# Kernel tuning notes

Hardware: AMD Instinct MI355X
Metric: run time of the kernel (lower is better)

## Reference

```python
import jax, jax.numpy as jnp
import numpy as np

K_H, K_W = 3, 3
STRIDE, PAD = 1, 1
GN_GROUPS = 32
EPS = 1e-5


def setup_inputs() -> dict:
    key = jax.random.key(0)
    k1, k2, k3 = jax.random.split(key, 3)
    B, C, H, W = 4, 256, 64, 64
    Cout = 256
    x = jax.random.normal(k1, (B, C, H, W), jnp.float32)
    offset = jax.random.normal(k2, (B, 2 * K_H * K_W, H, W), jnp.float32)
    weight = jax.random.normal(k3, (Cout, C, K_H, K_W), jnp.float32) * 0.02
    gamma = jnp.ones((Cout,), jnp.float32)
    beta = jnp.zeros((Cout,), jnp.float32)
    return {"x": x, "offset": offset, "weight": weight, "gamma": gamma, "beta": beta}


def _deform_conv(x, offset, weight):
    B, C, H, W = x.shape
    Cout = weight.shape[0]
    K = K_H * K_W
    Ho = (H + 2 * PAD - K_H) // STRIDE + 1
    Wo = (W + 2 * PAD - K_W) // STRIDE + 1
    ky, kx = jnp.meshgrid(jnp.arange(K_H), jnp.arange(K_W), indexing='ij')
    ky = ky.reshape(K).astype(x.dtype)
    kx = kx.reshape(K).astype(x.dtype)
    # base sampling positions per kernel tap
    py_base = (jnp.arange(Ho) * STRIDE - PAD).astype(x.dtype)[None, :] + ky[:, None]  # [K,Ho]
    px_base = (jnp.arange(Wo) * STRIDE - PAD).astype(x.dtype)[None, :] + kx[:, None]  # [K,Wo]
    off = offset.reshape(B, K, 2, Ho, Wo)  # mmcv layout: (dy, dx) pairs per tap
    py = py_base[None, :, :, None] + off[:, :, 0]  # [B,K,Ho,Wo]
    px = px_base[None, :, None, :] + off[:, :, 1]  # [B,K,Ho,Wo]
    y0 = jnp.floor(py)
    x0 = jnp.floor(px)
    ly = py - y0
    lx = px - x0
    xf = x.reshape(B, C, H * W)

    def gather(yi, xi):
        valid = (yi >= 0) & (yi <= H - 1) & (xi >= 0) & (xi <= W - 1)
        yc = jnp.clip(yi, 0, H - 1).astype(jnp.int32)
        xc = jnp.clip(xi, 0, W - 1).astype(jnp.int32)
        idx = yc * W + xc  # [B,K,Ho,Wo]
        vals = jax.vmap(lambda xb, ib: xb[:, ib])(xf, idx)  # [B,C,K,Ho,Wo]
        return vals * valid[:, None].astype(x.dtype)

    g00 = gather(y0, x0)
    g01 = gather(y0, x0 + 1)
    g10 = gather(y0 + 1, x0)
    g11 = gather(y0 + 1, x0 + 1)
    wy = ly[:, None]  # [B,1,K,Ho,Wo]
    wx = lx[:, None]
    val = ((1 - wy) * (1 - wx) * g00 + (1 - wy) * wx * g01
           + wy * (1 - wx) * g10 + wy * wx * g11)  # [B,C,K,Ho,Wo]
    return jnp.einsum('bckhw,ock->bohw', val, weight.reshape(Cout, C, K))


def reference(x, offset, weight, gamma, beta):
    y = _deform_conv(x, offset, weight)  # [B,Cout,Ho,Wo]
    B, C, H, W = y.shape
    yg = y.reshape(B, GN_GROUPS, C // GN_GROUPS, H, W)
    mean = jnp.mean(yg, axis=(2, 3, 4), keepdims=True)
    var = jnp.var(yg, axis=(2, 3, 4), keepdims=True)
    yn = ((yg - mean) * jax.lax.rsqrt(var + EPS)).reshape(B, C, H, W)
    out = yn * gamma[None, :, None, None] + beta[None, :, None, None]
    return jax.nn.relu(out)
```

## Files before the change

### kernel.cpp

```cpp
#include <hip/hip_runtime.h>

typedef unsigned short ushort_t;
typedef __bf16 bf16x8 __attribute__((ext_vector_type(8)));
typedef float f32x4 __attribute__((ext_vector_type(4)));
typedef void __attribute__((address_space(1))) gvoid_t;
typedef void __attribute__((address_space(3))) lvoid_t;

__device__ __forceinline__ float bflo(unsigned u) { return __builtin_bit_cast(float, u << 16); }
__device__ __forceinline__ float bfhi(unsigned u) { return __builtin_bit_cast(float, u & 0xffff0000u); }
__device__ __forceinline__ unsigned f2bf_bits(float f) {
  unsigned u = __builtin_bit_cast(unsigned, f);
  return (u + 0x7fffu + ((u >> 16) & 1u)) >> 16;
}
__device__ __forceinline__ ushort_t f2bf(float f) { return (ushort_t)f2bf_bits(f); }

#define VMWAIT(N) asm volatile("s_waitcnt vmcnt(" #N ")" ::: "memory")
#define LGKM0 asm volatile("s_waitcnt lgkmcnt(0)" ::: "memory")

__global__ __launch_bounds__(256) void k_prep_w(const float* __restrict__ w,
                                                ushort_t* __restrict__ wb) {
  const int idx = blockIdx.x * 256 + threadIdx.x;
  const float* src = w + (size_t)idx * 9;
  #pragma unroll
  for (int k = 0; k < 9; ++k)
    wb[(k << 16) + idx] = f2bf(src[k]);
}

__global__ __launch_bounds__(256) void k_prep_x(const float* __restrict__ x,
                                                ushort_t* __restrict__ xt) {
  __shared__ ushort_t tile[64][68];
  const int bid = blockIdx.x;
  const int b = bid >> 8;
  const int ct = (bid >> 6) & 3;
  const int pt = bid & 63;
  const int t = threadIdx.x;
  const float* xb = x + ((size_t)(b * 256 + ct * 64)) * 4096 + pt * 64;
  #pragma unroll
  for (int i = 0; i < 16; ++i) {
    const int idx = t + 256 * i;
    const int c_l = idx >> 6, p_l = idx & 63;
    tile[c_l][p_l] = f2bf(xb[(size_t)c_l * 4096 + p_l]);
  }
  __syncthreads();
  ushort_t* xo = xt + ((size_t)(b * 4096 + pt * 64)) * 256 + ct * 64;
  #pragma unroll
  for (int i = 0; i < 16; ++i) {
    const int idx = t + 256 * i;
    const int p_l = idx >> 6, c_l = idx & 63;
    xo[(size_t)p_l * 256 + c_l] = tile[c_l][p_l];
  }
}

struct SMeta {
  float w00, w01, w10, w11;
  int i00, i01, i10, i11;
};
__device__ __forceinline__ SMeta meta_for(int h, int gw, int k, float oy, float ox) {
  SMeta m;
  const float py = (float)(h - 1 + k / 3) + oy;
  const float px = (float)(gw - 1 + k % 3) + ox;
  const float fy = floorf(py), fx = floorf(px);
  const float ly = py - fy, lx = px - fx;
  const int iy0 = (int)fy, ix0 = (int)fx;
  const float vy0 = (iy0 >= 0 && iy0 < 64) ? 1.f : 0.f;
  const float vy1 = (iy0 >= -1 && iy0 < 63) ? 1.f : 0.f;
  const float vx0 = (ix0 >= 0 && ix0 < 64) ? 1.f : 0.f;
  const float vx1 = (ix0 >= -1 && ix0 < 63) ? 1.f : 0.f;
  m.w00 = (1.f - ly) * (1.f - lx) * vy0 * vx0;
  m.w01 = (1.f - ly) * lx * vy0 * vx1;
  m.w10 = ly * (1.f - lx) * vy1 * vx0;
  m.w11 = ly * lx * vy1 * vx1;
  const int cy0 = min(max(iy0, 0), 63), cy1 = min(max(iy0 + 1, 0), 63);
  const int cx0 = min(max(ix0, 0), 63), cx1 = min(max(ix0 + 1, 0), 63);
  m.i00 = (cy0 * 64 + cx0) * 256;
  m.i01 = (cy0 * 64 + cx1) * 256;
  m.i10 = (cy1 * 64 + cx0) * 256;
  m.i11 = (cy1 * 64 + cx1) * 256;
  return m;
}

__device__ __forceinline__ unsigned lerp_pack(unsigned a, unsigned b, unsigned c, unsigned d,
                                              float w00, float w01, float w10, float w11) {
  float lo = w00 * bflo(a) + w01 * bflo(b) + w10 * bflo(c) + w11 * bflo(d);
  float hi = w00 * bfhi(a) + w01 * bfhi(b) + w10 * bfhi(c) + w11 * bfhi(d);
  return f2bf_bits(lo) | (f2bf_bits(hi) << 16);
}

__global__ __launch_bounds__(512) void k_gemm(const float* __restrict__ off,
                                              const ushort_t* __restrict__ xt,
                                              const ushort_t* __restrict__ wb,
                                              float* __restrict__ y,
                                              float* __restrict__ stats) {
  __shared__ __attribute__((aligned(16))) ushort_t Abuf[2][64 * 64];
  __shared__ __attribute__((aligned(16))) ushort_t Bbuf[3][256 * 64];

  const int bid = blockIdx.x;
  const int lb = ((bid & 7) << 5) | (bid >> 3);
  const int b = lb >> 6;
  const int h = lb & 63;
  const int t = threadIdx.x;
  const int wave = t >> 6;
  const int lane = t & 63;
  const int wq = lane >> 4;
  const int wr = lane & 15;
  const int wm = wave >> 2;
  const int wn = wave & 3;

  const int s_w = t >> 3;
  const int c8 = t & 7;

  const f32x4 zero = {0.f, 0.f, 0.f, 0.f};
  f32x4 acc[2][4];
  #pragma unroll
  for (int i = 0; i < 2; ++i)
    #pragma unroll
    for (int j = 0; j < 4; ++j) acc[i][j] = zero;

  const ushort_t* xtb = xt + (size_t)b * 4096 * 256;

  float oy[9], ox[9];
  {
    const float* offb = off + (size_t)b * 18 * 4096 + h * 64 + s_w;
    #pragma unroll
    for (int k = 0; k < 9; ++k) {
      oy[k] = offb[(2 * k) * 4096];
      ox[k] = offb[(2 * k + 1) * 4096];
    }
  }

#define GATHER_ISSUE(TAP, C0)                             \
  {                                                       \
    m = meta_for(h, s_w, (TAP), oy[(TAP)], ox[(TAP)]);    \
    const int cc = (C0) + c8 * 8;                         \
    q00 = *(const uint4*)(xtb + m.i00 + cc);              \
    q01 = *(const uint4*)(xtb + m.i01 + cc);              \
    q10 = *(const uint4*)(xtb + m.i10 + cc);              \
    q11 = *(const uint4*)(xtb + m.i11 + cc);              \
  }

#define B_ISSUE(TAP, C0, BUF)                                                                \
  {                                                                                          \
    _Pragma("unroll") for (int i_ = 0; i_ < 4; ++i_) {                                       \
      const int idx_ = i_ * 512 + t;                                                         \
      const int row_ = idx_ >> 3, slot_ = idx_ & 7;                                          \
      const ushort_t* g_ = wb + ((TAP) << 16) + row_ * 256 + (C0) + ((slot_ ^ (row_ & 7)) << 3); \
      __builtin_amdgcn_global_load_lds((gvoid_t*)g_,                                         \
                                       (lvoid_t*)((char*)&Bbuf[(BUF)][0] + idx_ * 16), 16,   \
                                       0, 0);                                                \
    }                                                                                        \
  }

#define A_WRITE(BUF)                                                         \
  {                                                                          \
    uint4 r;                                                                 \
    r.x = lerp_pack(q00.x, q01.x, q10.x, q11.x, m.w00, m.w01, m.w10, m.w11); \
    r.y = lerp_pack(q00.y, q01.y, q10.y, q11.y, m.w00, m.w01, m.w10, m.w11); \
    r.z = lerp_pack(q00.z, q01.z, q10.z, q11.z, m.w00, m.w01, m.w10, m.w11); \
    r.w = lerp_pack(q00.w, q01.w, q10.w, q11.w, m.w00, m.w01, m.w10, m.w11); \
    *(uint4*)&Abuf[(BUF)][s_w * 64 + ((c8 ^ (s_w & 7)) << 3)] = r;           \
  }

  {
    uint4 q00, q01, q10, q11;
    SMeta m;
    GATHER_ISSUE(0, 0);
    B_ISSUE(0, 0, 0);
    B_ISSUE(0, 64, 1);
    VMWAIT(8);
    A_WRITE(0);
    LGKM0;
    __builtin_amdgcn_s_barrier();
  }

  #pragma unroll
  for (int n = 0; n < 36; ++n) {
    const int curB = n % 3;
    const int curA = n & 1;
    uint4 q00, q01, q10, q11;
    SMeta m;
    if (n < 35) {
      GATHER_ISSUE((n + 1) >> 2, ((n + 1) & 3) << 6);
    }
    if (n < 34) {
      B_ISSUE((n + 2) >> 2, ((n + 2) & 3) << 6, (n + 2) % 3);
    }
    VMWAIT(12);
    #pragma unroll
    for (int ks = 0; ks < 2; ++ks) {
      bf16x8 af[2], bfr[4];
      #pragma unroll
      for (int tm = 0; tm < 2; ++tm) {
        const int row = wm * 32 + tm * 16 + wr;
        const int slot = (ks * 4 + wq) ^ (row & 7);
        af[tm] = *(const bf16x8*)&Abuf[curA][row * 64 + slot * 8];
      }
      #pragma unroll
      for (int tn = 0; tn < 4; ++tn) {
        const int row = wn * 64 + tn * 16 + wr;
        const int slot = (ks * 4 + wq) ^ (row & 7);
        bfr[tn] = *(const bf16x8*)&Bbuf[curB][row * 64 + slot * 8];
      }
      #pragma unroll
      for (int tm = 0; tm < 2; ++tm)
        #pragma unroll
        for (int tn = 0; tn < 4; ++tn)
          acc[tm][tn] =
              __builtin_amdgcn_mfma_f32_16x16x32_bf16(af[tm], bfr[tn], acc[tm][tn], 0, 0, 0);
    }
    if (n < 35) {
      if (n == 34) {
        VMWAIT(0);
      } else {
        VMWAIT(4);
      }
      A_WRITE((n + 1) & 1);
      LGKM0;
      __builtin_amdgcn_s_barrier();
    }
  }
#undef GATHER_ISSUE
#undef B_ISSUE
#undef A_WRITE

  float* yb = y + ((size_t)(b * 4096 + h * 64)) * 256;
  #pragma unroll
  for (int tm = 0; tm < 2; ++tm) {
    #pragma unroll
    for (int tn = 0; tn < 4; ++tn) {
      const int o = wn * 64 + tn * 16 + wr;
      #pragma unroll
      for (int r2 = 0; r2 < 4; ++r2) {
        const int ww = wm * 32 + tm * 16 + wq * 4 + r2;
        yb[ww * 256 + o] = acc[tm][tn][r2];
      }
    }
  }
  #pragma unroll
  for (int tn = 0; tn < 4; ++tn) {
    float sum = 0.f, ss = 0.f;
    #pragma unroll
    for (int tm = 0; tm < 2; ++tm)
      #pragma unroll
      for (int r2 = 0; r2 < 4; ++r2) {
        const float v = acc[tm][tn][r2];
        sum += v;
        ss += v * v;
      }
    sum += __shfl_xor(sum, 16, 64);
    ss += __shfl_xor(ss, 16, 64);
    sum += __shfl_xor(sum, 32, 64);
    ss += __shfl_xor(ss, 32, 64);
    #pragma unroll
    for (int d = 1; d < 8; d <<= 1) {
      sum += __shfl_xor(sum, d, 64);
      ss += __shfl_xor(ss, d, 64);
    }
    if (wq == 0 && (wr & 7) == 0) {
      const int gi = wn * 8 + tn * 2 + (wr >> 3);
      atomicAdd(&stats[(b * 32 + gi) * 2], sum);
      atomicAdd(&stats[(b * 32 + gi) * 2 + 1], ss);
    }
  }
}

__global__ __launch_bounds__(256) void k_apply(const float* __restrict__ y,
                                               const float* __restrict__ stats,
                                               const float* __restrict__ gamma,
                                               const float* __restrict__ beta,
                                               float* __restrict__ out) {
  __shared__ float tile[64][65];
  __shared__ float sm[8], sr[8], sg[64], sb[64];
  const int bid = blockIdx.x;
  const int lb = ((bid & 7) << 7) | (bid >> 3);
  const int b = lb >> 8;
  const int st = (lb >> 2) & 63;
  const int ot = lb & 3;
  const int t = threadIdx.x;
  if (t < 8) {
    const int g = ot * 8 + t;
    const float s1 = stats[(b * 32 + g) * 2];
    const float s2 = stats[(b * 32 + g) * 2 + 1];
    const float mean = s1 * (1.f / 32768.f);
    const float var = s2 * (1.f / 32768.f) - mean * mean;
    sm[t] = mean;
    sr[t] = rsqrtf(var + 1e-5f);
  }
  if (t < 64) {
    sg[t] = gamma[ot * 64 + t];
    sb[t] = beta[ot * 64 + t];
  }
  const float* yb = y + ((size_t)(b * 4096 + st * 64)) * 256 + ot * 64;
  #pragma unroll
  for (int i = 0; i < 16; ++i) {
    const int idx = t + 256 * i;
    const int s_l = idx >> 6, o_l = idx & 63;
    tile[s_l][o_l] = yb[(size_t)s_l * 256 + o_l];
  }
  __syncthreads();
  float* ob = out + ((size_t)(b * 256 + ot * 64)) * 4096 + st * 64;
  #pragma unroll
  for (int i = 0; i < 16; ++i) {
    const int idx = t + 256 * i;
    const int o_l = idx >> 6, s_l = idx & 63;
    const int g = o_l >> 3;
    float v = (tile[s_l][o_l] - sm[g]) * sr[g] * sg[o_l] + sb[o_l];
    v = v > 0.f ? v : 0.f;
    ob[(size_t)o_l * 4096 + s_l] = v;
  }
}

extern "C" void kernel_launch(void* const* d_in, const int* in_sizes, int n_in,
                              void* d_out, int out_size, void* d_ws, size_t ws_size,
                              hipStream_t stream) {
  const float* x = (const float*)d_in[0];
  const float* off = (const float*)d_in[1];
  const float* w = (const float*)d_in[2];
  const float* gamma = (const float*)d_in[3];
  const float* beta = (const float*)d_in[4];
  float* out = (float*)d_out;

  char* ws = (char*)d_ws;
  float* y = (float*)(ws);
  ushort_t* xt = (ushort_t*)(ws + 16777216);
  ushort_t* wb = (ushort_t*)(ws + 25165824);
  float* stats = (float*)(ws + 26345472);

  hipMemsetAsync(stats, 0, 1024, stream);
  k_prep_w<<<256, 256, 0, stream>>>(w, wb);
  k_prep_x<<<1024, 256, 0, stream>>>(x, xt);
  k_gemm<<<256, 512, 0, stream>>>(off, xt, wb, y, stats);
  k_apply<<<1024, 256, 0, stream>>>(y, stats, gamma, beta, out);
}
```

Before: 93.75 us.

## Split GEMM row tile in half to launch twice as many blocks

Each GEMM block now handles 32 output pixels instead of 64 (half an image row), so the grid doubles from 256 to 512 blocks, one per MI355X CU-ish slot. Only half the threads do the bilinear gather. The B weight pipeline drops from triple to double buffering with prefetch distance one, and MFMA sections get raised wave priority. This lowers LDS use and raises occupancy and CU coverage, at the cost of loading every weight tile twice as often overall and less arithmetic per B load.

```diff
diff --git a/kernel.cpp b/kernel.cpp
--- a/kernel.cpp
+++ b/kernel.cpp
@@ -91,13 +91,14 @@
                                               const ushort_t* __restrict__ wb,
                                               float* __restrict__ y,
                                               float* __restrict__ stats) {
-  __shared__ __attribute__((aligned(16))) ushort_t Abuf[2][64 * 64];
-  __shared__ __attribute__((aligned(16))) ushort_t Bbuf[3][256 * 64];
+  __shared__ __attribute__((aligned(16))) ushort_t Abuf[2][32 * 64];
+  __shared__ __attribute__((aligned(16))) ushort_t Bbuf[2][256 * 64];
 
   const int bid = blockIdx.x;
-  const int lb = ((bid & 7) << 5) | (bid >> 3);
-  const int b = lb >> 6;
-  const int h = lb & 63;
+  const int lb = ((bid & 7) << 6) | (bid >> 3);
+  const int b = lb >> 7;
+  const int h = (lb >> 1) & 63;
+  const int wh = lb & 1;
   const int t = threadIdx.x;
   const int wave = t >> 6;
   const int lane = t & 63;
@@ -105,22 +106,22 @@
   const int wr = lane & 15;
   const int wm = wave >> 2;
   const int wn = wave & 3;
-
-  const int s_w = t >> 3;
+  const bool samp = (t < 256);
+
+  const int s_w = (t >> 3) & 31;
   const int c8 = t & 7;
+  const int gw = wh * 32 + s_w;
 
   const f32x4 zero = {0.f, 0.f, 0.f, 0.f};
-  f32x4 acc[2][4];
-  #pragma unroll
-  for (int i = 0; i < 2; ++i)
-    #pragma unroll
-    for (int j = 0; j < 4; ++j) acc[i][j] = zero;
+  f32x4 acc[4];
+  #pragma unroll
+  for (int j = 0; j < 4; ++j) acc[j] = zero;
 
   const ushort_t* xtb = xt + (size_t)b * 4096 * 256;
 
   float oy[9], ox[9];
-  {
-    const float* offb = off + (size_t)b * 18 * 4096 + h * 64 + s_w;
+  if (samp) {
+    const float* offb = off + (size_t)b * 18 * 4096 + h * 64 + gw;
     #pragma unroll
     for (int k = 0; k < 9; ++k) {
       oy[k] = offb[(2 * k) * 4096];
@@ -128,14 +129,14 @@
     }
   }
 
-#define GATHER_ISSUE(TAP, C0)                             \
-  {                                                       \
-    m = meta_for(h, s_w, (TAP), oy[(TAP)], ox[(TAP)]);    \
-    const int cc = (C0) + c8 * 8;                         \
-    q00 = *(const uint4*)(xtb + m.i00 + cc);              \
-    q01 = *(const uint4*)(xtb + m.i01 + cc);              \
-    q10 = *(const uint4*)(xtb + m.i10 + cc);              \
-    q11 = *(const uint4*)(xtb + m.i11 + cc);              \
+#define GATHER_ISSUE(TAP, C0)                           \
+  {                                                     \
+    m = meta_for(h, gw, (TAP), oy[(TAP)], ox[(TAP)]);   \
+    const int cc = (C0) + c8 * 8;                       \
+    q00 = *(const uint4*)(xtb + m.i00 + cc);            \
+    q01 = *(const uint4*)(xtb + m.i01 + cc);            \
+    q10 = *(const uint4*)(xtb + m.i10 + cc);            \
+    q11 = *(const uint4*)(xtb + m.i11 + cc);            \
   }
 
 #define B_ISSUE(TAP, C0, BUF)                                                                \
@@ -163,57 +164,62 @@
   {
     uint4 q00, q01, q10, q11;
     SMeta m;
-    GATHER_ISSUE(0, 0);
+    if (samp) {
+      GATHER_ISSUE(0, 0);
+    }
     B_ISSUE(0, 0, 0);
-    B_ISSUE(0, 64, 1);
-    VMWAIT(8);
-    A_WRITE(0);
+    if (samp) {
+      VMWAIT(4);
+      A_WRITE(0);
+    }
     LGKM0;
     __builtin_amdgcn_s_barrier();
   }
 
   #pragma unroll
   for (int n = 0; n < 36; ++n) {
-    const int curB = n % 3;
-    const int curA = n & 1;
+    const int cur = n & 1;
+    const int nb = cur ^ 1;
     uint4 q00, q01, q10, q11;
     SMeta m;
     if (n < 35) {
-      GATHER_ISSUE((n + 1) >> 2, ((n + 1) & 3) << 6);
-    }
-    if (n < 34) {
-      B_ISSUE((n + 2) >> 2, ((n + 2) & 3) << 6, (n + 2) % 3);
-    }
-    VMWAIT(12);
+      if (samp) {
+        GATHER_ISSUE((n + 1) >> 2, ((n + 1) & 3) << 6);
+      }
+      B_ISSUE((n + 1) >> 2, ((n + 1) & 3) << 6, nb);
+      if (samp) {
+        VMWAIT(8);
+      } else {
+        VMWAIT(4);
+      }
+    } else {
+      VMWAIT(0);
+    }
     #pragma unroll
     for (int ks = 0; ks < 2; ++ks) {
-      bf16x8 af[2], bfr[4];
-      #pragma unroll
-      for (int tm = 0; tm < 2; ++tm) {
-        const int row = wm * 32 + tm * 16 + wr;
+      bf16x8 af, bfr[4];
+      {
+        const int row = wm * 16 + wr;
         const int slot = (ks * 4 + wq) ^ (row & 7);
-        af[tm] = *(const bf16x8*)&Abuf[curA][row * 64 + slot * 8];
+        af = *(const bf16x8*)&Abuf[cur][row * 64 + slot * 8];
       }
       #pragma unroll
       for (int tn = 0; tn < 4; ++tn) {
         const int row = wn * 64 + tn * 16 + wr;
         const int slot = (ks * 4 + wq) ^ (row & 7);
-        bfr[tn] = *(const bf16x8*)&Bbuf[curB][row * 64 + slot * 8];
+        bfr[tn] = *(const bf16x8*)&Bbuf[cur][row * 64 + slot * 8];
       }
+      __builtin_amdgcn_s_setprio(1);
       #pragma unroll
-      for (int tm = 0; tm < 2; ++tm)
-        #pragma unroll
-        for (int tn = 0; tn < 4; ++tn)
-          acc[tm][tn] =
-              __builtin_amdgcn_mfma_f32_16x16x32_bf16(af[tm], bfr[tn], acc[tm][tn], 0, 0, 0);
+      for (int tn = 0; tn < 4; ++tn)
+        acc[tn] = __builtin_amdgcn_mfma_f32_16x16x32_bf16(af, bfr[tn], acc[tn], 0, 0, 0);
+      __builtin_amdgcn_s_setprio(0);
+    }
+    if (n < 35 && samp) {
+      VMWAIT(4);
+      A_WRITE(nb);
     }
     if (n < 35) {
-      if (n == 34) {
-        VMWAIT(0);
-      } else {
-        VMWAIT(4);
-      }
-      A_WRITE((n + 1) & 1);
       LGKM0;
       __builtin_amdgcn_s_barrier();
     }
@@ -222,30 +228,25 @@
 #undef B_ISSUE
 #undef A_WRITE
 
-  float* yb = y + ((size_t)(b * 4096 + h * 64)) * 256;
-  #pragma unroll
-  for (int tm = 0; tm < 2; ++tm) {
-    #pragma unroll
-    for (int tn = 0; tn < 4; ++tn) {
-      const int o = wn * 64 + tn * 16 + wr;
-      #pragma unroll
-      for (int r2 = 0; r2 < 4; ++r2) {
-        const int ww = wm * 32 + tm * 16 + wq * 4 + r2;
-        yb[ww * 256 + o] = acc[tm][tn][r2];
-      }
+  float* yb = y + ((size_t)(b * 4096 + h * 64 + wh * 32)) * 256;
+  #pragma unroll
+  for (int tn = 0; tn < 4; ++tn) {
+    const int o = wn * 64 + tn * 16 + wr;
+    #pragma unroll
+    for (int r2 = 0; r2 < 4; ++r2) {
+      const int ww = wm * 16 + wq * 4 + r2;
+      yb[ww * 256 + o] = acc[tn][r2];
     }
   }
   #pragma unroll
   for (int tn = 0; tn < 4; ++tn) {
     float sum = 0.f, ss = 0.f;
     #pragma unroll
-    for (int tm = 0; tm < 2; ++tm)
-      #pragma unroll
-      for (int r2 = 0; r2 < 4; ++r2) {
-        const float v = acc[tm][tn][r2];
-        sum += v;
-        ss += v * v;
-      }
+    for (int r2 = 0; r2 < 4; ++r2) {
+      const float v = acc[tn][r2];
+      sum += v;
+      ss += v * v;
+    }
     sum += __shfl_xor(sum, 16, 64);
     ss += __shfl_xor(ss, 16, 64);
     sum += __shfl_xor(sum, 32, 64);
@@ -328,6 +329,6 @@
   hipMemsetAsync(stats, 0, 1024, stream);
   k_prep_w<<<256, 256, 0, stream>>>(w, wb);
   k_prep_x<<<1024, 256, 0, stream>>>(x, xt);
-  k_gemm<<<256, 512, 0, stream>>>(off, xt, wb, y, stats);
+  k_gemm<<<512, 512, 0, stream>>>(off, xt, wb, y, stats);
   k_apply<<<1024, 256, 0, stream>>>(y, stats, gamma, beta, out);
 }
```

Result: slower. 113.0 us (+20.5%).

## Prefetch bilinear gather two K-steps ahead with double-buffered registers

Applied to the files above, without the earlier changes.

Moves the deformable bilinear gather loads from one iteration ahead to two iterations ahead, matching the weight-tile prefetch distance. It uses two register sets for the four corner loads and their sampling metadata. The vmcnt waits are reordered to the top of each iteration so the gather results have a full MFMA step to arrive before the lerp and LDS write. The aim is to hide global gather latency behind matrix work, at the cost of roughly doubling the registers held for in-flight gather data, which may lower occupancy or cause spills.

```diff
diff --git a/kernel.cpp b/kernel.cpp
--- a/kernel.cpp
+++ b/kernel.cpp
@@ -128,14 +128,17 @@
     }
   }
 
-#define GATHER_ISSUE(TAP, C0)                             \
-  {                                                       \
-    m = meta_for(h, s_w, (TAP), oy[(TAP)], ox[(TAP)]);    \
-    const int cc = (C0) + c8 * 8;                         \
-    q00 = *(const uint4*)(xtb + m.i00 + cc);              \
-    q01 = *(const uint4*)(xtb + m.i01 + cc);              \
-    q10 = *(const uint4*)(xtb + m.i10 + cc);              \
-    q11 = *(const uint4*)(xtb + m.i11 + cc);              \
+  uint4 q00s[2], q01s[2], q10s[2], q11s[2];
+  SMeta ms[2];
+
+#define GATHER_ISSUE(TAP, C0, SET)                              \
+  {                                                             \
+    ms[SET] = meta_for(h, s_w, (TAP), oy[(TAP)], ox[(TAP)]);    \
+    const int cc = (C0) + c8 * 8;                               \
+    q00s[SET] = *(const uint4*)(xtb + ms[SET].i00 + cc);        \
+    q01s[SET] = *(const uint4*)(xtb + ms[SET].i01 + cc);        \
+    q10s[SET] = *(const uint4*)(xtb + ms[SET].i10 + cc);        \
+    q11s[SET] = *(const uint4*)(xtb + ms[SET].i11 + cc);        \
   }
 
 #define B_ISSUE(TAP, C0, BUF)                                                                \
@@ -150,41 +153,45 @@
     }                                                                                        \
   }
 
-#define A_WRITE(BUF)                                                         \
-  {                                                                          \
-    uint4 r;                                                                 \
-    r.x = lerp_pack(q00.x, q01.x, q10.x, q11.x, m.w00, m.w01, m.w10, m.w11); \
-    r.y = lerp_pack(q00.y, q01.y, q10.y, q11.y, m.w00, m.w01, m.w10, m.w11); \
-    r.z = lerp_pack(q00.z, q01.z, q10.z, q11.z, m.w00, m.w01, m.w10, m.w11); \
-    r.w = lerp_pack(q00.w, q01.w, q10.w, q11.w, m.w00, m.w01, m.w10, m.w11); \
-    *(uint4*)&Abuf[(BUF)][s_w * 64 + ((c8 ^ (s_w & 7)) << 3)] = r;           \
+#define A_WRITE(SET, BUF)                                                         \
+  {                                                                               \
+    uint4 r;                                                                      \
+    r.x = lerp_pack(q00s[SET].x, q01s[SET].x, q10s[SET].x, q11s[SET].x,           \
+                    ms[SET].w00, ms[SET].w01, ms[SET].w10, ms[SET].w11);          \
+    r.y = lerp_pack(q00s[SET].y, q01s[SET].y, q10s[SET].y, q11s[SET].y,           \
+                    ms[SET].w00, ms[SET].w01, ms[SET].w10, ms[SET].w11);          \
+    r.z = lerp_pack(q00s[SET].z, q01s[SET].z, q10s[SET].z, q11s[SET].z,           \
+                    ms[SET].w00, ms[SET].w01, ms[SET].w10, ms[SET].w11);          \
+    r.w = lerp_pack(q00s[SET].w, q01s[SET].w, q10s[SET].w, q11s[SET].w,           \
+                    ms[SET].w00, ms[SET].w01, ms[SET].w10, ms[SET].w11);          \
+    *(uint4*)&Abuf[(BUF)][s_w * 64 + ((c8 ^ (s_w & 7)) << 3)] = r;                \
   }
 
   {
-    uint4 q00, q01, q10, q11;
-    SMeta m;
-    GATHER_ISSUE(0, 0);
+    GATHER_ISSUE(0, 0, 0);
     B_ISSUE(0, 0, 0);
+    GATHER_ISSUE(0, 64, 1);
     B_ISSUE(0, 64, 1);
-    VMWAIT(8);
-    A_WRITE(0);
+    VMWAIT(12);
+    A_WRITE(0, 0);
     LGKM0;
     __builtin_amdgcn_s_barrier();
   }
 
   #pragma unroll
   for (int n = 0; n < 36; ++n) {
+    const int curA = n & 1;
+    const int nbA = curA ^ 1;
     const int curB = n % 3;
-    const int curA = n & 1;
-    uint4 q00, q01, q10, q11;
-    SMeta m;
-    if (n < 35) {
-      GATHER_ISSUE((n + 1) >> 2, ((n + 1) & 3) << 6);
-    }
-    if (n < 34) {
+    if (n == 35) {
+      VMWAIT(0);
+    } else {
+      VMWAIT(4);
+    }
+    if (n <= 33) {
+      GATHER_ISSUE((n + 2) >> 2, ((n + 2) & 3) << 6, curA);
       B_ISSUE((n + 2) >> 2, ((n + 2) & 3) << 6, (n + 2) % 3);
     }
-    VMWAIT(12);
     #pragma unroll
     for (int ks = 0; ks < 2; ++ks) {
       bf16x8 af[2], bfr[4];
@@ -208,12 +215,7 @@
               __builtin_amdgcn_mfma_f32_16x16x32_bf16(af[tm], bfr[tn], acc[tm][tn], 0, 0, 0);
     }
     if (n < 35) {
-      if (n == 34) {
-        VMWAIT(0);
-      } else {
-        VMWAIT(4);
-      }
-      A_WRITE((n + 1) & 1);
+      A_WRITE(nbA, nbA);
       LGKM0;
       __builtin_amdgcn_s_barrier();
     }
```

After: 87.33 us. 1.07x faster.

## Double K-step to 128 channels with two-stage gather and weight pipeline

Applied to the files above, without the earlier changes.

Restructures the deformable-conv GEMM main loop from 36 steps of 64 channels to 18 steps of 128 channels. A and B tiles are double-buffered with two 64-channel halves each. Bilinear gathers are now issued one step further ahead, and weight tiles are loaded only one step ahead instead of two. The goal is to halve the number of barriers and waits per tile and to hide gather latency better. The cost is more registers (eight uint4 gather vectors in flight) and more LDS (2x2x4K for A plus 2x2x16K for B), which may cut occupancy and reduce how far weight loads run ahead.

```diff
diff --git a/kernel.cpp b/kernel.cpp
--- a/kernel.cpp
+++ b/kernel.cpp
@@ -91,8 +91,8 @@
                                               const ushort_t* __restrict__ wb,
                                               float* __restrict__ y,
                                               float* __restrict__ stats) {
-  __shared__ __attribute__((aligned(16))) ushort_t Abuf[2][64 * 64];
-  __shared__ __attribute__((aligned(16))) ushort_t Bbuf[3][256 * 64];
+  __shared__ __attribute__((aligned(16))) ushort_t Abuf[2][2][64 * 64];
+  __shared__ __attribute__((aligned(16))) ushort_t Bbuf[2][2][256 * 64];
 
   const int bid = blockIdx.x;
   const int lb = ((bid & 7) << 5) | (bid >> 3);
@@ -128,77 +128,89 @@
     }
   }
 
+  SMeta mg;
+  uint4 qa00, qa01, qa10, qa11;
+  uint4 qb00, qb01, qb10, qb11;
+
 #define GATHER_ISSUE(TAP, C0)                             \
   {                                                       \
-    m = meta_for(h, s_w, (TAP), oy[(TAP)], ox[(TAP)]);    \
+    mg = meta_for(h, s_w, (TAP), oy[(TAP)], ox[(TAP)]);   \
     const int cc = (C0) + c8 * 8;                         \
-    q00 = *(const uint4*)(xtb + m.i00 + cc);              \
-    q01 = *(const uint4*)(xtb + m.i01 + cc);              \
-    q10 = *(const uint4*)(xtb + m.i10 + cc);              \
-    q11 = *(const uint4*)(xtb + m.i11 + cc);              \
-  }
-
-#define B_ISSUE(TAP, C0, BUF)                                                                \
-  {                                                                                          \
-    _Pragma("unroll") for (int i_ = 0; i_ < 4; ++i_) {                                       \
-      const int idx_ = i_ * 512 + t;                                                         \
-      const int row_ = idx_ >> 3, slot_ = idx_ & 7;                                          \
-      const ushort_t* g_ = wb + ((TAP) << 16) + row_ * 256 + (C0) + ((slot_ ^ (row_ & 7)) << 3); \
-      __builtin_amdgcn_global_load_lds((gvoid_t*)g_,                                         \
-                                       (lvoid_t*)((char*)&Bbuf[(BUF)][0] + idx_ * 16), 16,   \
-                                       0, 0);                                                \
-    }                                                                                        \
-  }
-
-#define A_WRITE(BUF)                                                         \
-  {                                                                          \
-    uint4 r;                                                                 \
-    r.x = lerp_pack(q00.x, q01.x, q10.x, q11.x, m.w00, m.w01, m.w10, m.w11); \
-    r.y = lerp_pack(q00.y, q01.y, q10.y, q11.y, m.w00, m.w01, m.w10, m.w11); \
-    r.z = lerp_pack(q00.z, q01.z, q10.z, q11.z, m.w00, m.w01, m.w10, m.w11); \
-    r.w = lerp_pack(q00.w, q01.w, q10.w, q11.w, m.w00, m.w01, m.w10, m.w11); \
-    *(uint4*)&Abuf[(BUF)][s_w * 64 + ((c8 ^ (s_w & 7)) << 3)] = r;           \
+    qa00 = *(const uint4*)(xtb + mg.i00 + cc);            \
+    qa01 = *(const uint4*)(xtb + mg.i01 + cc);            \
+    qa10 = *(const uint4*)(xtb + mg.i10 + cc);            \
+    qa11 = *(const uint4*)(xtb + mg.i11 + cc);            \
+    qb00 = *(const uint4*)(xtb + mg.i00 + cc + 64);       \
+    qb01 = *(const uint4*)(xtb + mg.i01 + cc + 64);       \
+    qb10 = *(const uint4*)(xtb + mg.i10 + cc + 64);       \
+    qb11 = *(const uint4*)(xtb + mg.i11 + cc + 64);       \
+  }
+
+#define B_ISSUE(TAP, C0, PB)                                                                   \
+  {                                                                                            \
+    _Pragma("unroll") for (int ch_ = 0; ch_ < 2; ++ch_) {                                      \
+      _Pragma("unroll") for (int i_ = 0; i_ < 4; ++i_) {                                       \
+        const int idx_ = i_ * 512 + t;                                                         \
+        const int row_ = idx_ >> 3, slot_ = idx_ & 7;                                          \
+        const ushort_t* g_ =                                                                   \
+            wb + ((TAP) << 16) + row_ * 256 + (C0) + ch_ * 64 + ((slot_ ^ (row_ & 7)) << 3);   \
+        __builtin_amdgcn_global_load_lds((gvoid_t*)g_,                                         \
+                                         (lvoid_t*)((char*)&Bbuf[(PB)][ch_][0] + idx_ * 16),   \
+                                         16, 0, 0);                                            \
+      }                                                                                        \
+    }                                                                                          \
+  }
+
+#define A_WRITE(PB)                                                                  \
+  {                                                                                  \
+    uint4 r;                                                                         \
+    r.x = lerp_pack(qa00.x, qa01.x, qa10.x, qa11.x, mg.w00, mg.w01, mg.w10, mg.w11); \
+    r.y = lerp_pack(qa00.y, qa01.y, qa10.y, qa11.y, mg.w00, mg.w01, mg.w10, mg.w11); \
+    r.z = lerp_pack(qa00.z, qa01.z, qa10.z, qa11.z, mg.w00, mg.w01, mg.w10, mg.w11); \
+    r.w = lerp_pack(qa00.w, qa01.w, qa10.w, qa11.w, mg.w00, mg.w01, mg.w10, mg.w11); \
+    *(uint4*)&Abuf[(PB)][0][s_w * 64 + ((c8 ^ (s_w & 7)) << 3)] = r;                 \
+    r.x = lerp_pack(qb00.x, qb01.x, qb10.x, qb11.x, mg.w00, mg.w01, mg.w10, mg.w11); \
+    r.y = lerp_pack(qb00.y, qb01.y, qb10.y, qb11.y, mg.w00, mg.w01, mg.w10, mg.w11); \
+    r.z = lerp_pack(qb00.z, qb01.z, qb10.z, qb11.z, mg.w00, mg.w01, mg.w10, mg.w11); \
+    r.w = lerp_pack(qb00.w, qb01.w, qb10.w, qb11.w, mg.w00, mg.w01, mg.w10, mg.w11); \
+    *(uint4*)&Abuf[(PB)][1][s_w * 64 + ((c8 ^ (s_w & 7)) << 3)] = r;                 \
   }
 
   {
-    uint4 q00, q01, q10, q11;
-    SMeta m;
     GATHER_ISSUE(0, 0);
     B_ISSUE(0, 0, 0);
-    B_ISSUE(0, 64, 1);
+    A_WRITE(0);
+    GATHER_ISSUE(0, 128);
     VMWAIT(8);
-    A_WRITE(0);
     LGKM0;
     __builtin_amdgcn_s_barrier();
   }
 
   #pragma unroll
-  for (int n = 0; n < 36; ++n) {
-    const int curB = n % 3;
-    const int curA = n & 1;
-    uint4 q00, q01, q10, q11;
-    SMeta m;
-    if (n < 35) {
-      GATHER_ISSUE((n + 1) >> 2, ((n + 1) & 3) << 6);
-    }
-    if (n < 34) {
-      B_ISSUE((n + 2) >> 2, ((n + 2) & 3) << 6, (n + 2) % 3);
-    }
-    VMWAIT(12);
-    #pragma unroll
-    for (int ks = 0; ks < 2; ++ks) {
+  for (int p = 0; p < 18; ++p) {
+    const int pb = p & 1;
+    const int nb = pb ^ 1;
+    if (p < 17) {
+      const int tap1 = (p + 1) >> 1;
+      const int c01 = ((p + 1) & 1) << 7;
+      B_ISSUE(tap1, c01, nb);
+    }
+    #pragma unroll
+    for (int ks = 0; ks < 4; ++ks) {
+      const int ch = ks >> 1;
+      const int kk = ks & 1;
       bf16x8 af[2], bfr[4];
       #pragma unroll
       for (int tm = 0; tm < 2; ++tm) {
         const int row = wm * 32 + tm * 16 + wr;
-        const int slot = (ks * 4 + wq) ^ (row & 7);
-        af[tm] = *(const bf16x8*)&Abuf[curA][row * 64 + slot * 8];
+        const int slot = (kk * 4 + wq) ^ (row & 7);
+        af[tm] = *(const bf16x8*)&Abuf[pb][ch][row * 64 + slot * 8];
       }
       #pragma unroll
       for (int tn = 0; tn < 4; ++tn) {
         const int row = wn * 64 + tn * 16 + wr;
-        const int slot = (ks * 4 + wq) ^ (row & 7);
-        bfr[tn] = *(const bf16x8*)&Bbuf[curB][row * 64 + slot * 8];
+        const int slot = (kk * 4 + wq) ^ (row & 7);
+        bfr[tn] = *(const bf16x8*)&Bbuf[pb][ch][row * 64 + slot * 8];
       }
       #pragma unroll
       for (int tm = 0; tm < 2; ++tm)
@@ -207,13 +219,16 @@
           acc[tm][tn] =
               __builtin_amdgcn_mfma_f32_16x16x32_bf16(af[tm], bfr[tn], acc[tm][tn], 0, 0, 0);
     }
-    if (n < 35) {
-      if (n == 34) {
+    if (p < 17) {
+      A_WRITE(nb);
+      if (p < 16) {
+        const int tap2 = (p + 2) >> 1;
+        const int c02 = ((p + 2) & 1) << 7;
+        GATHER_ISSUE(tap2, c02);
+        VMWAIT(8);
+      } else {
         VMWAIT(0);
-      } else {
-        VMWAIT(4);
-      }
-      A_WRITE((n + 1) & 1);
+      }
       LGKM0;
       __builtin_amdgcn_s_barrier();
     }
```

Result: faster. 83.74 us (-10.7%).
